# Performance work log

Measured on AMD Instinct MI355X. Metric: run time of the kernel, lower is better.

## Reference

```python
import jax, jax.numpy as jnp
import numpy as np
from jax import lax

EPS = 1e-5

def _conv(x, w, b, stride):
    y = lax.conv_general_dilated(x, w, window_strides=(stride, stride), padding='VALID',
                                 dimension_numbers=('NCHW', 'OIHW', 'NCHW'))
    return y + b[None, :, None, None]

def _upsample_zero(x, s):
    B, C, H, W = x.shape
    z = jnp.zeros((B, C, H * s, W * s), dtype=x.dtype)
    return z.at[:, :, ::s, ::s].set(x)

def setup_inputs() -> dict:
    key = jax.random.key(0)
    ks = jax.random.split(key, 12)
    B, C, H, W = 512, 3, 128, 128
    FLAT = 3 * 65 * 65  # 12675 per the shape chain
    sc = lambda fan_in: 1.0 / np.sqrt(fan_in)
    return {
        'x': jax.random.normal(ks[0], (B, C, H, W), dtype=jnp.float32),
        'bn_gamma': jnp.ones((C,), jnp.float32),
        'bn_beta': jnp.zeros((C,), jnp.float32),
        'w1': jax.random.normal(ks[1], (3, 3, 5, 5), jnp.float32) * sc(3 * 25),
        'b1': jax.random.normal(ks[2], (3,), jnp.float32) * 0.01,
        'w2': jax.random.normal(ks[3], (3, 3, 5, 5), jnp.float32) * sc(3 * 25),
        'b2': jax.random.normal(ks[4], (3,), jnp.float32) * 0.01,
        'fc1_w': jax.random.normal(ks[5], (128, FLAT), jnp.float32) * sc(FLAT),
        'fc1_b': jnp.zeros((128,), jnp.float32),
        'fc2_w': jax.random.normal(ks[6], (10, 128), jnp.float32) * sc(128),
        'fc2_b': jnpp if False else jnp.zeros((10,), jnp.float32),
    }

def reference(x, bn_gamma, bn_beta, w1, b1, w2, b2, fc1_w, fc1_b, fc2_w, fc2_b):
    # BatchNorm1d over active sites (= all original pixels; zero-pad sites are inactive)
    mean = x.mean(axis=(0, 2, 3))
    var = ((x - mean[None, :, None, None]) ** 2).mean(axis=(0, 2, 3))  # biased, as torch BN
    xn = (x - mean[None, :, None, None]) * lax.rsqrt(var + EPS)[None, :, None, None]
    xn = xn * bn_gamma[None, :, None, None] + bn_beta[None, :, None, None]
    # SparseZeroPad2d(1) -> [B,3,130,130]
    h = jnp.pad(xn, ((0, 0), (0, 0), (1, 1), (1, 1)))
    # cv1 (k5,s5) -> [B,3,26,26]; SparseScale2d(5) -> zeros interleaved [B,3,130,130]
    h = _upsample_zero(_conv(h, w1, b1, 5), 5)
    h = jax.nn.relu(h)
    # cv2 (k5,s5) -> [B,3,26,26]; scale -> [B,3,130,130]
    h = _upsample_zero(_conv(h, w2, b2, 5), 5)
    h = jax.nn.relu(h)
    # SparseMaxPool2d(2,2) -> [B,3,65,65]; features >= 0 so dense pool matches sparse pool
    h = lax.reduce_window(h, -jnp.inf, lax.max, (1, 1, 2, 2), (1, 1, 2, 2), 'VALID')
    # flatten -> dropout(eval=identity) -> fc1 -> relu -> fc2 -> log_softmax
    f = h.reshape(h.shape[0], -1)
    f = jax.nn.relu(f @ fc1_w.T + fc1_b)
    logits = f @ fc2_w.T + fc2_b
    return jax.nn.log_softmax(logits, axis=1)
```

## Files before the change

kernel.cpp:

```cpp
#include <hip/hip_runtime.h>

#define BN_EPS 1e-5f

typedef short short8 __attribute__((ext_vector_type(8)));
typedef float f32x4 __attribute__((ext_vector_type(4)));
typedef unsigned short ushort;

__device__ inline ushort f2bf(float f) {
  unsigned int u = __float_as_uint(f);
  u += 0x7FFFu + ((u >> 16) & 1u);
  return (ushort)(u >> 16);
}


#define NPOS 346112
#define LROW 144

__global__ __launch_bounds__(256) void k_convraw(
    const float* __restrict__ x,
    const float* __restrict__ w1g,
    float* __restrict__ S,
    float* __restrict__ psumS)
{
  __shared__ float s_xp[130 * LROW];
  __shared__ float red[4][6];
  const int tid = threadIdx.x;
  const int b = blockIdx.x;

  for (int i = tid; i < 2 * LROW; i += 256) {
    int r = (i < LROW) ? 0 : 129;
    int c = (i < LROW) ? i : i - LROW;
    s_xp[r * LROW + c] = 0.f;
  }
  if (tid < 128) {
    s_xp[(tid + 1) * LROW + 3] = 0.f;
    s_xp[(tid + 1) * LROW + 132] = 0.f;
  }

  float st_s[3], st_q[3];

  #pragma unroll
  for (int c = 0; c < 3; c++) {
    if (c) __syncthreads();

    const float4* xp = (const float4*)(x + ((size_t)b * 3 + c) * 16384);
    float s = 0.f, q = 0.f;
    #pragma unroll
    for (int i = 0; i < 16; i++) {
      float4 a4 = xp[i * 256 + tid];
      int idx = (i * 256 + tid) << 2;
      int r = idx >> 7, col = idx & 127;
      float* d = &s_xp[(r + 1) * LROW + col + 4];
      d[0] = a4.x; d[1] = a4.y; d[2] = a4.z; d[3] = a4.w;
      s += (a4.x + a4.y) + (a4.z + a4.w);
      q += (a4.x * a4.x + a4.y * a4.y) + (a4.z * a4.z + a4.w * a4.w);
    }
    st_s[c] = s; st_q[c] = q;
    __syncthreads();

    #pragma unroll
    for (int pp = 0; pp < 3; pp++) {
      int pos = tid + pp * 256;
      if (pos < 676) {
        int oy = pos / 26, ox = pos - oy * 26;
        const float* base = &s_xp[(5 * oy) * LROW + 5 * ox + 3];
        float a0 = 0.f, a1 = 0.f, a2 = 0.f;
        #pragma unroll
        for (int ky = 0; ky < 5; ky++) {
          #pragma unroll
          for (int kx = 0; kx < 5; kx++) {
            float v = base[ky * LROW + kx];
            a0 += w1g[0 * 75 + c * 25 + ky * 5 + kx] * v;
            a1 += w1g[1 * 75 + c * 25 + ky * 5 + kx] * v;
            a2 += w1g[2 * 75 + c * 25 + ky * 5 + kx] * v;
          }
        }
        size_t gp = (size_t)b * 676 + pos;
        S[(size_t)(c * 3 + 0) * NPOS + gp] = a0;
        S[(size_t)(c * 3 + 1) * NPOS + gp] = a1;
        S[(size_t)(c * 3 + 2) * NPOS + gp] = a2;
      }
    }
  }

  #pragma unroll
  for (int off = 32; off; off >>= 1) {
    #pragma unroll
    for (int c = 0; c < 3; c++) {
      st_s[c] += __shfl_down(st_s[c], off);
      st_q[c] += __shfl_down(st_q[c], off);
    }
  }
  __syncthreads();
  int lane = tid & 63, wv = tid >> 6;
  if (lane == 0) {
    red[wv][0] = st_s[0]; red[wv][1] = st_s[1]; red[wv][2] = st_s[2];
    red[wv][3] = st_q[0]; red[wv][4] = st_q[1]; red[wv][5] = st_q[2];
  }
  __syncthreads();
  if (tid < 6)
    psumS[tid * 512 + b] = (red[0][tid] + red[1][tid]) + (red[2][tid] + red[3][tid]);
}

__global__ __launch_bounds__(384) void k_reduce(const float* __restrict__ psumS,
                                                float* __restrict__ stats) {
  int w = threadIdx.x >> 6, lane = threadIdx.x & 63;
  const float* src = psumS + w * 512;
  float acc = 0.f;
  #pragma unroll
  for (int k = 0; k < 8; k++) acc += src[lane + 64 * k];
  #pragma unroll
  for (int off = 32; off; off >>= 1) acc += __shfl_down(acc, off);
  if (lane == 0) stats[w] = acc;
}

__device__ inline float gval(const float* __restrict__ row, int k) {
  if (k >= 2028) return 0.f;
  int c = k / 676;
  int rem = k - c * 676;
  int oy = rem / 26, ox = rem - oy * 26;
  int col = c * 4225 + ((5 * oy) >> 1) * 65 + ((5 * ox) >> 1);
  return row[col];
}

__global__ __launch_bounds__(256) void k_gather(const float* __restrict__ fc1_w,
                                                ushort* __restrict__ WgtB) {
  int gid = blockIdx.x * 256 + threadIdx.x;
  int l = gid & 63;
  int n = ((gid >> 12) << 4) + (l & 15);
  int kbase = (((gid >> 6) & 63) << 5) + ((l >> 4) << 3);
  const float* row = fc1_w + n * 12675;
  uint4 o;
  unsigned int w[4];
  #pragma unroll
  for (int i = 0; i < 4; i++) {
    ushort lo = f2bf(gval(row, kbase + 2 * i));
    ushort hi = f2bf(gval(row, kbase + 2 * i + 1));
    w[i] = (unsigned int)lo | ((unsigned int)hi << 16);
  }
  o.x = w[0]; o.y = w[1]; o.z = w[2]; o.w = w[3];
  ((uint4*)WgtB)[gid] = o;
}

__global__ __launch_bounds__(256) void k_combine(
    const float* __restrict__ S,
    const float* __restrict__ stats,
    const float* __restrict__ gamma, const float* __restrict__ beta,
    const float* __restrict__ w1, const float* __restrict__ b1,
    const float* __restrict__ w2, const float* __restrict__ b2,
    ushort* __restrict__ featB)
{
  __shared__ float s_w1[225];
  __shared__ float s_w2[9];
  __shared__ float s_scale[3], s_shift[3], s_b1[3], s_b2[3];
  __shared__ float s_T[9][9];
  const int tid = threadIdx.x;
  if (tid < 225) s_w1[tid] = w1[tid];
  if (tid < 9) s_w2[tid] = w2[tid * 25];
  if (tid < 3) {
    const float N = 512.f * 128.f * 128.f;
    float mean = stats[tid] / N;
    float var = stats[3 + tid] / N - mean * mean;
    float sc = gamma[tid] * rsqrtf(var + BN_EPS);
    s_scale[tid] = sc;
    s_shift[tid] = beta[tid] - mean * sc;
    s_b1[tid] = b1[tid];
    s_b2[tid] = b2[tid];
  }
  __syncthreads();
  if (tid < 81) {
    int cls = tid / 9, oc = tid - (tid / 9) * 9;
    int rcl = cls / 3, ccl = cls - rcl * 3;
    int o = oc / 3, c = oc - o * 3;
    int ky0 = (rcl == 0) ? 1 : 0, ky1 = (rcl == 2) ? 3 : 4;
    int kx0 = (ccl == 0) ? 1 : 0, kx1 = (ccl == 2) ? 3 : 4;
    float t = 0.f;
    for (int ky = ky0; ky <= ky1; ky++)
      for (int kx = kx0; kx <= kx1; kx++)
        t += s_w1[o * 75 + c * 25 + ky * 5 + kx];
    s_T[cls][oc] = t;
  }
  __syncthreads();

  int gpos = blockIdx.x * 256 + tid;
  int b = gpos / 676;
  int pos = gpos - b * 676;
  int oy = pos / 26, ox = pos - oy * 26;
  int rcl = (oy == 0) ? 0 : ((oy == 25) ? 2 : 1);
  int ccl = (ox == 0) ? 0 : ((ox == 25) ? 2 : 1);
  int cls = rcl * 3 + ccl;

  float h[3];
  #pragma unroll
  for (int o = 0; o < 3; o++) {
    float a = s_b1[o];
    #pragma unroll
    for (int c = 0; c < 3; c++) {
      a += s_scale[c] * S[(size_t)(c * 3 + o) * NPOS + gpos];
      a += s_shift[c] * s_T[cls][o * 3 + c];
    }
    h[o] = fmaxf(a, 0.f);
  }
  ushort* fb = featB + (size_t)b * 2048;
  #pragma unroll
  for (int o = 0; o < 3; o++) {
    float v = s_b2[o] + s_w2[3 * o] * h[0] + s_w2[3 * o + 1] * h[1] + s_w2[3 * o + 2] * h[2];
    fb[o * 676 + pos] = f2bf(fmaxf(v, 0.f));
  }
  if (pos < 20) fb[2028 + pos] = 0;
}

__global__ __launch_bounds__(512) void k_fc(
    const ushort* __restrict__ featB,
    const ushort* __restrict__ WgtB,
    const float* __restrict__ fc1_b,
    const float* __restrict__ fc2_w, const float* __restrict__ fc2_b,
    float* __restrict__ out)
{
  __shared__ float s_f[16][132];
  __shared__ float s_lg[16][10];
  const int tid = threadIdx.x;
  const int lane = tid & 63;
  const int t = tid >> 6;
  const int m0 = blockIdx.x * 16;

  const ushort* aptr = featB + (size_t)(m0 + (lane & 15)) * 2048 + ((lane >> 4) << 3);
  const ushort* bptr = WgtB + ((size_t)t * 4096 + lane) * 8;

  f32x4 acc = {0.f, 0.f, 0.f, 0.f};
  #pragma unroll 4
  for (int kk = 0; kk < 64; kk++) {
    short8 a = *(const short8*)(aptr + kk * 32);
    short8 bfr = *(const short8*)(bptr + kk * 512);
    acc = __builtin_amdgcn_mfma_f32_16x16x32_bf16(a, bfr, acc, 0, 0, 0);
  }
  {
    int n = t * 16 + (lane & 15);
    float bias = fc1_b[n];
    int mb = (lane >> 4) << 2;
    #pragma unroll
    for (int r = 0; r < 4; r++)
      s_f[mb + r][n] = fmaxf(acc[r] + bias, 0.f);
  }
  __syncthreads();

  if (tid < 160) {
    int m = tid & 15, q = tid >> 4;
    const float* wr = fc2_w + q * 128;
    float a2 = fc2_b[q];
    #pragma unroll 8
    for (int k = 0; k < 128; k++) a2 += wr[k] * s_f[m][k];
    s_lg[m][q] = a2;
  }
  __syncthreads();

  if (tid < 16) {
    float mx = s_lg[tid][0];
    #pragma unroll
    for (int q = 1; q < 10; q++) mx = fmaxf(mx, s_lg[tid][q]);
    float se = 0.f;
    #pragma unroll
    for (int q = 0; q < 10; q++) se += expf(s_lg[tid][q] - mx);
    float lse = mx + logf(se);
    float* op = out + (size_t)(m0 + tid) * 10;
    #pragma unroll
    for (int q = 0; q < 10; q++) op[q] = s_lg[tid][q] - lse;
  }
}

extern "C" void kernel_launch(void* const* d_in, const int* in_sizes, int n_in,
                              void* d_out, int out_size, void* d_ws, size_t ws_size,
                              hipStream_t stream) {
  const float* x      = (const float*)d_in[0];
  const float* gamma  = (const float*)d_in[1];
  const float* beta   = (const float*)d_in[2];
  const float* w1     = (const float*)d_in[3];
  const float* b1     = (const float*)d_in[4];
  const float* w2     = (const float*)d_in[5];
  const float* b2     = (const float*)d_in[6];
  const float* fc1_w  = (const float*)d_in[7];
  const float* fc1_b  = (const float*)d_in[8];
  const float* fc2_w  = (const float*)d_in[9];
  const float* fc2_b  = (const float*)d_in[10];
  float* out = (float*)d_out;
  float* wsf = (float*)d_ws;

  float* stats  = wsf;
  float* psumS  = wsf + 64;
  ushort* WgtB  = (ushort*)(wsf + 16384);
  ushort* featB = (ushort*)(wsf + 262144);
  float* S      = wsf + 786432;

  k_convraw<<<512, 256, 0, stream>>>(x, w1, S, psumS);
  k_gather<<<128, 256, 0, stream>>>(fc1_w, WgtB);
  k_reduce<<<1, 384, 0, stream>>>(psumS, stats);
  k_combine<<<1352, 256, 0, stream>>>(S, stats, gamma, beta, w1, b1, w2, b2, featB);
  k_fc<<<32, 512, 0, stream>>>(featB, WgtB, fc1_b, fc2_w, fc2_b, out);
}
```

Baseline: 60.07 us.

## Split raw conv kernel into per-channel half-image blocks for more parallelism

The first conv kernel is now launched with one block per (batch, channel, image half) instead of one block per batch image. This gives 3072 blocks instead of 512 and shrinks shared memory from 130 to 65 padded rows. That should improve occupancy and load balance across CUs and remove the serial channel loop. The partial statistics buffer doubles in length and the reduce kernel reads 16 chunks per stat, and each block now does less work in exchange for more launch/block overhead.

```diff
diff --git a/kernel.cpp b/kernel.cpp
--- a/kernel.cpp
+++ b/kernel.cpp
@@ -22,93 +22,83 @@
     float* __restrict__ S,
     float* __restrict__ psumS)
 {
-  __shared__ float s_xp[130 * LROW];
-  __shared__ float red[4][6];
+  __shared__ float s_xp[65 * LROW];
+  __shared__ float red[4][2];
   const int tid = threadIdx.x;
-  const int b = blockIdx.x;
-
-  for (int i = tid; i < 2 * LROW; i += 256) {
-    int r = (i < LROW) ? 0 : 129;
-    int c = (i < LROW) ? i : i - LROW;
-    s_xp[r * LROW + c] = 0.f;
-  }
-  if (tid < 128) {
-    s_xp[(tid + 1) * LROW + 3] = 0.f;
-    s_xp[(tid + 1) * LROW + 132] = 0.f;
-  }
-
-  float st_s[3], st_q[3];
-
-  #pragma unroll
-  for (int c = 0; c < 3; c++) {
-    if (c) __syncthreads();
-
-    const float4* xp = (const float4*)(x + ((size_t)b * 3 + c) * 16384);
-    float s = 0.f, q = 0.f;
-    #pragma unroll
-    for (int i = 0; i < 16; i++) {
-      float4 a4 = xp[i * 256 + tid];
-      int idx = (i * 256 + tid) << 2;
-      int r = idx >> 7, col = idx & 127;
-      float* d = &s_xp[(r + 1) * LROW + col + 4];
-      d[0] = a4.x; d[1] = a4.y; d[2] = a4.z; d[3] = a4.w;
-      s += (a4.x + a4.y) + (a4.z + a4.w);
-      q += (a4.x * a4.x + a4.y * a4.y) + (a4.z * a4.z + a4.w * a4.w);
+  const int bid = blockIdx.x;
+  const int h = bid & 1;
+  const int c = (bid >> 1) % 3;
+  const int b = bid / 6;
+
+  const int zrow = h ? 64 : 0;
+  for (int i = tid; i < LROW; i += 256) s_xp[zrow * LROW + i] = 0.f;
+  if (tid < 65) { s_xp[tid * LROW + 3] = 0.f; s_xp[tid * LROW + 132] = 0.f; }
+
+  const int r0 = h ? 64 : 0;
+  const int off0 = h ? 0 : 1;
+
+  const float4* xp = (const float4*)(x + ((size_t)b * 3 + c) * 16384 + (size_t)r0 * 128);
+  float s = 0.f, q = 0.f;
+  #pragma unroll
+  for (int i = 0; i < 8; i++) {
+    int v = i * 256 + tid;
+    float4 a4 = xp[v];
+    int lr = (v >> 5) + off0;
+    int col = (v & 31) << 2;
+    float* d = &s_xp[lr * LROW + col + 4];
+    d[0] = a4.x; d[1] = a4.y; d[2] = a4.z; d[3] = a4.w;
+    s += (a4.x + a4.y) + (a4.z + a4.w);
+    q += (a4.x * a4.x + a4.y * a4.y) + (a4.z * a4.z + a4.w * a4.w);
+  }
+  __syncthreads();
+
+  const float* wc = w1g + c * 25;
+  #pragma unroll
+  for (int pp = 0; pp < 2; pp++) {
+    int p = tid + pp * 256;
+    if (p < 338) {
+      int ol = p / 26, ox = p - ol * 26;
+      const float* base = &s_xp[(5 * ol) * LROW + 5 * ox + 3];
+      float a0 = 0.f, a1 = 0.f, a2 = 0.f;
+      #pragma unroll
+      for (int ky = 0; ky < 5; ky++) {
+        #pragma unroll
+        for (int kx = 0; kx < 5; kx++) {
+          float v = base[ky * LROW + kx];
+          a0 += wc[ky * 5 + kx] * v;
+          a1 += wc[75 + ky * 5 + kx] * v;
+          a2 += wc[150 + ky * 5 + kx] * v;
+        }
+      }
+      int oy = h * 13 + ol;
+      size_t gp = (size_t)b * 676 + oy * 26 + ox;
+      S[(size_t)(c * 3 + 0) * NPOS + gp] = a0;
+      S[(size_t)(c * 3 + 1) * NPOS + gp] = a1;
+      S[(size_t)(c * 3 + 2) * NPOS + gp] = a2;
     }
-    st_s[c] = s; st_q[c] = q;
-    __syncthreads();
-
-    #pragma unroll
-    for (int pp = 0; pp < 3; pp++) {
-      int pos = tid + pp * 256;
-      if (pos < 676) {
-        int oy = pos / 26, ox = pos - oy * 26;
-        const float* base = &s_xp[(5 * oy) * LROW + 5 * ox + 3];
-        float a0 = 0.f, a1 = 0.f, a2 = 0.f;
-        #pragma unroll
-        for (int ky = 0; ky < 5; ky++) {
-          #pragma unroll
-          for (int kx = 0; kx < 5; kx++) {
-            float v = base[ky * LROW + kx];
-            a0 += w1g[0 * 75 + c * 25 + ky * 5 + kx] * v;
-            a1 += w1g[1 * 75 + c * 25 + ky * 5 + kx] * v;
-            a2 += w1g[2 * 75 + c * 25 + ky * 5 + kx] * v;
-          }
-        }
-        size_t gp = (size_t)b * 676 + pos;
-        S[(size_t)(c * 3 + 0) * NPOS + gp] = a0;
-        S[(size_t)(c * 3 + 1) * NPOS + gp] = a1;
-        S[(size_t)(c * 3 + 2) * NPOS + gp] = a2;
-      }
-    }
   }
 
   #pragma unroll
   for (int off = 32; off; off >>= 1) {
-    #pragma unroll
-    for (int c = 0; c < 3; c++) {
-      st_s[c] += __shfl_down(st_s[c], off);
-      st_q[c] += __shfl_down(st_q[c], off);
-    }
-  }
-  __syncthreads();
+    s += __shfl_down(s, off);
+    q += __shfl_down(q, off);
+  }
   int lane = tid & 63, wv = tid >> 6;
-  if (lane == 0) {
-    red[wv][0] = st_s[0]; red[wv][1] = st_s[1]; red[wv][2] = st_s[2];
-    red[wv][3] = st_q[0]; red[wv][4] = st_q[1]; red[wv][5] = st_q[2];
-  }
-  __syncthreads();
-  if (tid < 6)
-    psumS[tid * 512 + b] = (red[0][tid] + red[1][tid]) + (red[2][tid] + red[3][tid]);
+  if (lane == 0) { red[wv][0] = s; red[wv][1] = q; }
+  __syncthreads();
+  if (tid == 0)
+    psumS[c * 1024 + b * 2 + h] = (red[0][0] + red[1][0]) + (red[2][0] + red[3][0]);
+  if (tid == 1)
+    psumS[(3 + c) * 1024 + b * 2 + h] = (red[0][1] + red[1][1]) + (red[2][1] + red[3][1]);
 }
 
 __global__ __launch_bounds__(384) void k_reduce(const float* __restrict__ psumS,
                                                 float* __restrict__ stats) {
   int w = threadIdx.x >> 6, lane = threadIdx.x & 63;
-  const float* src = psumS + w * 512;
+  const float* src = psumS + w * 1024;
   float acc = 0.f;
   #pragma unroll
-  for (int k = 0; k < 8; k++) acc += src[lane + 64 * k];
+  for (int k = 0; k < 16; k++) acc += src[lane + 64 * k];
   #pragma unroll
   for (int off = 32; off; off >>= 1) acc += __shfl_down(acc, off);
   if (lane == 0) stats[w] = acc;
@@ -291,7 +281,7 @@
   ushort* featB = (ushort*)(wsf + 262144);
   float* S      = wsf + 786432;
 
-  k_convraw<<<512, 256, 0, stream>>>(x, w1, S, psumS);
+  k_convraw<<<3072, 256, 0, stream>>>(x, w1, S, psumS);
   k_gather<<<128, 256, 0, stream>>>(fc1_w, WgtB);
   k_reduce<<<1, 384, 0, stream>>>(psumS, stats);
   k_combine<<<1352, 256, 0, stream>>>(S, stats, gamma, beta, w1, b1, w2, b2, featB);
```

Measured after the change: 56.80 us. 1.06x faster.
